# Performance work log

Hardware: AMD Instinct MI355X
Metric: run time of the kernel (lower is better)

Reference implementation:

```python
import jax, jax.numpy as jnp
import numpy as np

N = 100000
E = 1600000
IN_DIM = 64
HID = 64
OUT = 64
NCLS = 40
EPS_BN = 1e-5


def _sym_norms(src, dst, n):
    # DGL GraphConv norm='both': src scaled by out_degree^-1/2, dst by in_degree^-1/2,
    # degrees clamped to min 1.
    ones = jnp.ones(src.shape[0], dtype=jnp.float32)
    deg_out = jax.ops.segment_sum(ones, src, num_segments=n)
    deg_in = jax.ops.segment_sum(ones, dst, num_segments=n)
    return jnp.clip(deg_out, 1.0) ** -0.5, jnp.clip(deg_in, 1.0) ** -0.5


def _graph_conv(x, src, dst, norm_src, norm_dst, W, b):
    # D_dst^{-1/2} A D_src^{-1/2} X W + b
    x = x * norm_src[:, None]
    agg = jax.ops.segment_sum(x[src], dst, num_segments=x.shape[0])
    agg = agg * norm_dst[:, None]
    return agg @ W + b


def _gcn(x, src, dst, W1, b1, W2, b2):
    ns, nd = _sym_norms(src, dst, x.shape[0])
    h = jax.nn.relu(_graph_conv(x, src, dst, ns, nd, W1, b1))
    return _graph_conv(h, src, dst, ns, nd, W2, b2)


def setup_inputs() -> dict:
    key = jax.random.key(0)
    ks = jax.random.split(key, 16)
    glorot = lambda k, fi, fo: jax.random.normal(k, (fi, fo), jnp.float32) * np.sqrt(2.0 / (fi + fo))
    return {
        "feat1": jax.random.normal(ks[0], (N, IN_DIM), jnp.float32),
        "src1": jax.random.randint(ks[1], (E,), 0, N, jnp.int32),
        "dst1": jax.random.randint(ks[2], (E,), 0, N, jnp.int32),
        "feat2": jax.random.normal(ks[3], (N, IN_DIM), jnp.float32),
        "src2": jax.random.randint(ks[4], (E,), 0, N, jnp.int32),
        "dst2": jax.random.randint(ks[5], (E,), 0, N, jnp.int32),
        "W1a": glorot(ks[6], IN_DIM, HID), "b1a": jnp.zeros(HID, jnp.float32),
        "W1b": glorot(ks[7], HID, OUT), "b1b": jnp.zeros(OUT, jnp.float32),
        "W2a": glorot(ks[8], IN_DIM, HID), "b2a": jnp.zeros(HID, jnp.float32),
        "W2b": glorot(ks[9], HID, OUT), "b2b": jnp.zeros(OUT, jnp.float32),
        "Wm1": glorot(ks[10], OUT, HID), "bm1": jnp.zeros(HID, jnp.float32),
        "gamma": jnp.ones(HID, jnp.float32), "beta": jnp.zeros(HID, jnp.float32),
        "Wm2": glorot(ks[11], HID, NCLS), "bm2": jnp.zeros(NCLS, jnp.float32),
    }


def reference(feat1, src1, dst1, feat2, src2, dst2,
              W1a, b1a, W1b, b1b, W2a, b2a, W2b, b2b,
              Wm1, bm1, gamma, beta, Wm2, bm2):
    h1 = _gcn(feat1, src1, dst1, W1a, b1a, W1b, b1b)
    h2 = _gcn(feat2, src2, dst2, W2a, b2a, W2b, b2b)
    # torch .std() is unbiased (ddof=1)
    z1 = (h1 - h1.mean(0)) / jnp.std(h1, axis=0, ddof=1)
    z2 = (h2 - h2.mean(0)) / jnp.std(h2, axis=0, ddof=1)
    z = (z1 + z2) * 0.5
    # MLP2 head: Linear -> BatchNorm1d (training-mode batch stats) -> ReLU -> Linear
    y = z @ Wm1 + bm1
    mu = y.mean(0)
    var = y.var(0)  # biased, as BN uses
    y = (y - mu) * jax.lax.rsqrt(var + EPS_BN) * gamma + beta
    pred_y = jax.nn.relu(y) @ Wm2 + bm2
    return (z1, z2, pred_y)
```

## Files before the change

kernel.cpp:

```cpp
#include <hip/hip_runtime.h>
#include <hip/hip_bf16.h>

#define DIM 64
#define NCLS_OUT 40
#define BSH 8
#define BROWS 256
#define BIN_CHUNK 12288

typedef __hip_bfloat16 bf16;

__device__ __forceinline__ float lane_bcast(float v, int l) {
  return __int_as_float(__builtin_amdgcn_readlane(__float_as_int(v), l));
}
__device__ __forceinline__ unsigned short f2bf_bits(float f) {
  bf16 h = __float2bfloat16(f);
  return *reinterpret_cast<unsigned short*>(&h);
}

__device__ __forceinline__ float ldf(const void* p, long i, int m) {
  return m ? ((const float*)p)[i] : __bfloat162float(((const bf16*)p)[i]);
}
__device__ __forceinline__ void stf(void* p, long i, float v, int m) {
  if (m) ((float*)p)[i] = v;
  else ((bf16*)p)[i] = __float2bfloat16(v);
}

__global__ void k_detect(const unsigned int* __restrict__ wds, int nw, int* __restrict__ mode) {
  __shared__ int cnt_s;
  if (threadIdx.x == 0) cnt_s = 0;
  __syncthreads();
  int c = 0;
  for (int i = threadIdx.x; i < nw; i += 1024) {
    unsigned h = wds[i] & 0xFFFFu;
    unsigned e = (h >> 7) & 0xFFu;
    if (e == 0xFFu || (e != 0u && e < 0x60u)) c++;
  }
  atomicAdd(&cnt_s, c);
  __syncthreads();
  if (threadIdx.x == 0) *mode = (cnt_s > nw / 16) ? 1 : 0;
}

__global__ void k_deg_hist(const int* __restrict__ src1, const int* __restrict__ dst1,
                           const int* __restrict__ src2, const int* __restrict__ dst2,
                           int* __restrict__ deg, int* __restrict__ bh,
                           int n, int e1, int etot, int NB) {
  extern __shared__ int cnt[];
  for (int b = threadIdx.x; b < NB; b += blockDim.x) cnt[b] = 0;
  __syncthreads();
  int stride = gridDim.x * blockDim.x;
  for (int i = blockIdx.x * blockDim.x + threadIdx.x; i < etot; i += stride) {
    int s, row;
    if (i < e1) { s = src1[i]; row = dst1[i]; }
    else { s = src2[i - e1]; row = n + dst2[i - e1]; }
    atomicAdd(&deg[2 * n + (row < n ? 0 : 0) + (i < e1 ? s : n + s)], 1);
    atomicAdd(&cnt[row >> BSH], 1);
  }
  __syncthreads();
  for (int b = threadIdx.x; b < NB; b += blockDim.x)
    if (cnt[b]) atomicAdd(&bh[b], cnt[b]);
}

__global__ void k_norm(const int* __restrict__ deg, float* __restrict__ nrm, int n4) {
  int i = blockIdx.x * 256 + threadIdx.x;
  if (i < n4) {
    int d = deg[i];
    if (d < 1) d = 1;
    nrm[i] = rsqrtf((float)d);
  }
}

__global__ void k_bscan(const int* __restrict__ bh, int* __restrict__ bbase,
                        int* __restrict__ gcur, int* __restrict__ rp,
                        int NB, int etot, int n2) {
  __shared__ int sm[256];
  __shared__ int carry_s;
  int t = threadIdx.x;
  if (t == 0) carry_s = 0;
  __syncthreads();
  for (int base = 0; base < NB; base += 256) {
    int i = base + t;
    int v = (i < NB) ? bh[i] : 0;
    sm[t] = v;
    __syncthreads();
    for (int o = 1; o < 256; o <<= 1) {
      int a = (t >= o) ? sm[t - o] : 0;
      __syncthreads();
      sm[t] += a;
      __syncthreads();
    }
    int c = carry_s;
    int excl = c + sm[t] - v;
    int tot = sm[255];
    __syncthreads();
    if (i < NB) { bbase[i] = excl; gcur[i] = excl; }
    if (t == 0) carry_s = c + tot;
    __syncthreads();
  }
  if (t == 0) { bbase[NB] = etot; rp[n2] = etot; }
}

__global__ void __launch_bounds__(256) k_bin(
    const int* __restrict__ src1, const int* __restrict__ dst1,
    const int* __restrict__ src2, const int* __restrict__ dst2,
    int* __restrict__ gcur, unsigned* __restrict__ eb,
    int n, int e1, int etot, int NB) {
  extern __shared__ int lds[];
  int* cnt = lds;
  int* base = lds + NB;
  int t = threadIdx.x;
  int c0 = blockIdx.x * BIN_CHUNK;
  int cend = c0 + BIN_CHUNK;
  if (cend > etot) cend = etot;
  for (int b = t; b < NB; b += 256) cnt[b] = 0;
  __syncthreads();
  for (int i = c0 + t; i < cend; i += 256) {
    int row = (i < e1) ? dst1[i] : (n + dst2[i - e1]);
    atomicAdd(&cnt[row >> BSH], 1);
  }
  __syncthreads();
  for (int b = t; b < NB; b += 256) {
    int c = cnt[b];
    base[b] = c ? atomicAdd(&gcur[b], c) : 0;
    cnt[b] = 0;
  }
  __syncthreads();
  for (int i = c0 + t; i < cend; i += 256) {
    int s, row;
    if (i < e1) { s = src1[i]; row = dst1[i]; }
    else { s = src2[i - e1]; row = n + dst2[i - e1]; }
    int b = row >> BSH;
    int l = atomicAdd(&cnt[b], 1);
    eb[base[b] + l] = ((unsigned)(row & (BROWS - 1)) << 24) | (unsigned)s;
  }
}

__global__ void __launch_bounds__(256) k_fine(
    const unsigned* __restrict__ eb, const int* __restrict__ bbase,
    int* __restrict__ rp, int* __restrict__ deg, int* __restrict__ sb,
    int n2, int NB) {
  __shared__ int hist[256];
  __shared__ int sm[256];
  __shared__ int curs[256];
  int t = threadIdx.x;
  for (int b = blockIdx.x; b < NB; b += gridDim.x) {
    int ebeg = bbase[b], eend = bbase[b + 1];
    hist[t] = 0;
    __syncthreads();
    for (int i = ebeg + t; i < eend; i += 256)
      atomicAdd(&hist[eb[i] >> 24], 1);
    __syncthreads();
    int v = hist[t];
    sm[t] = v;
    __syncthreads();
    for (int o = 1; o < 256; o <<= 1) {
      int a = (t >= o) ? sm[t - o] : 0;
      __syncthreads();
      sm[t] += a;
      __syncthreads();
    }
    int excl = sm[t] - v;
    int row = (b << BSH) + t;
    if (row < n2) { deg[row] = v; rp[row] = ebeg + excl; }
    curs[t] = excl;
    __syncthreads();
    for (int i = ebeg + t; i < eend; i += 256) {
      unsigned u = eb[i];
      int l = atomicAdd(&curs[u >> 24], 1);
      sb[ebeg + l] = (int)(u & 0xFFFFFFu);
    }
    __syncthreads();
  }
}

__global__ void k_scale_all(const void* __restrict__ f1, const void* __restrict__ f2,
                            const float* __restrict__ norms, bf16* __restrict__ P,
                            int n, const int* __restrict__ mode) {
  int m = *mode;
  int i = blockIdx.x * 256 + threadIdx.x;
  int nd = n * DIM;
  if (i >= 2 * nd) return;
  int g = i >= nd;
  int li = g ? i - nd : i;
  float ns = norms[2 * n + g * n + (li >> 6)];
  P[i] = __float2bfloat16(ldf(g ? f2 : f1, li, m) * ns);
}

__global__ void k_scale_one(const void* __restrict__ f, const float* __restrict__ ns,
                            bf16* __restrict__ P, int nd, const int* __restrict__ mode) {
  int m = *mode;
  int i = blockIdx.x * 256 + threadIdx.x;
  if (i < nd) P[i] = __float2bfloat16(ldf(f, i, m) * ns[i >> 6]);
}

__global__ void __launch_bounds__(256) k_gmm(
    const bf16* __restrict__ X, const int* __restrict__ rp, const int* __restrict__ sb,
    const void* __restrict__ Wg0, const void* __restrict__ bg0,
    const void* __restrict__ Wg1, const void* __restrict__ bg1,
    const float* __restrict__ pre0, const float* __restrict__ pre1,
    const float* __restrict__ post0, const float* __restrict__ post1,
    bf16* __restrict__ Y, int n, int relu, const int* __restrict__ mode,
    int dual, int gsel, float* __restrict__ stats) {
  int m = *mode;
  int t = threadIdx.x, lane = t & 63, wid = t >> 6;
  int g = dual ? (blockIdx.x & 1) : gsel;
  int ord = dual ? (blockIdx.x >> 1) : blockIdx.x;
  int nblk = dual ? (gridDim.x >> 1) : gridDim.x;
  int rowbase = dual ? g * n : 0;

  const void* W = g ? Wg1 : Wg0;
  const void* bb = g ? bg1 : bg0;
  const float* pre = g ? pre1 : pre0;
  const float* post = g ? post1 : post0;

  unsigned wp[32];
#pragma unroll
  for (int i = 0; i < 32; ++i) {
    unsigned lb = f2bf_bits(ldf(W, (2 * i) * 64 + lane, m));
    unsigned hb = f2bf_bits(ldf(W, (2 * i + 1) * 64 + lane, m));
    wp[i] = lb | (hb << 16);
  }
  float bias = ldf(bb, lane, m);
  float ps = 0.f, pq = 0.f;

  int stride = nblk * 4;
  for (int node = ord * 4 + wid; node < n; node += stride) {
    int b0 = rp[g * n + node], e0 = rp[g * n + node + 1];
    float a0 = 0.f, a1 = 0.f, a2 = 0.f, a3 = 0.f;
    for (int base = b0; base < e0; base += 64) {
      int cnt = e0 - base;
      if (cnt > 64) cnt = 64;
      int eidx = (lane < cnt) ? sb[base + lane] : 0;
      int j = 0;
      for (; j + 8 <= cnt; j += 8) {
        int s0 = __builtin_amdgcn_readlane(eidx, j);
        int s1 = __builtin_amdgcn_readlane(eidx, j + 1);
        int s2 = __builtin_amdgcn_readlane(eidx, j + 2);
        int s3 = __builtin_amdgcn_readlane(eidx, j + 3);
        int s4 = __builtin_amdgcn_readlane(eidx, j + 4);
        int s5 = __builtin_amdgcn_readlane(eidx, j + 5);
        int s6 = __builtin_amdgcn_readlane(eidx, j + 6);
        int s7 = __builtin_amdgcn_readlane(eidx, j + 7);
        float v0 = __bfloat162float(X[(long)(rowbase + s0) * DIM + lane]);
        float v1 = __bfloat162float(X[(long)(rowbase + s1) * DIM + lane]);
        float v2 = __bfloat162float(X[(long)(rowbase + s2) * DIM + lane]);
        float v3 = __bfloat162float(X[(long)(rowbase + s3) * DIM + lane]);
        float v4 = __bfloat162float(X[(long)(rowbase + s4) * DIM + lane]);
        float v5 = __bfloat162float(X[(long)(rowbase + s5) * DIM + lane]);
        float v6 = __bfloat162float(X[(long)(rowbase + s6) * DIM + lane]);
        float v7 = __bfloat162float(X[(long)(rowbase + s7) * DIM + lane]);
        a0 += v0; a1 += v1; a2 += v2; a3 += v3;
        a0 += v4; a1 += v5; a2 += v6; a3 += v7;
      }
      for (; j + 4 <= cnt; j += 4) {
        int s0 = __builtin_amdgcn_readlane(eidx, j);
        int s1 = __builtin_amdgcn_readlane(eidx, j + 1);
        int s2 = __builtin_amdgcn_readlane(eidx, j + 2);
        int s3 = __builtin_amdgcn_readlane(eidx, j + 3);
        a0 += __bfloat162float(X[(long)(rowbase + s0) * DIM + lane]);
        a1 += __bfloat162float(X[(long)(rowbase + s1) * DIM + lane]);
        a2 += __bfloat162float(X[(long)(rowbase + s2) * DIM + lane]);
        a3 += __bfloat162float(X[(long)(rowbase + s3) * DIM + lane]);
      }
      for (; j < cnt; ++j) {
        int s0 = __builtin_amdgcn_readlane(eidx, j);
        a0 += __bfloat162float(X[(long)(rowbase + s0) * DIM + lane]);
      }
    }
    float acc = (a0 + a1) + (a2 + a3);
    acc *= pre[node];
    float r = 0.f;
#pragma unroll
    for (int i = 0; i < 32; ++i) {
      r = fmaf(lane_bcast(acc, 2 * i), __uint_as_float(wp[i] << 16), r);
      r = fmaf(lane_bcast(acc, 2 * i + 1), __uint_as_float(wp[i] & 0xFFFF0000u), r);
    }
    r += bias;
    if (relu) r = fmaxf(r, 0.f);
    if (post) r *= post[node];
    Y[(long)(rowbase + node) * DIM + lane] = __float2bfloat16(r);
    ps += r;
    pq += r * r;
  }

  if (stats) {
    __shared__ float ssum[4][64], ssq[4][64];
    ssum[wid][lane] = ps;
    ssq[wid][lane] = pq;
    __syncthreads();
    if (t < 64) {
      float a = ssum[0][t] + ssum[1][t] + ssum[2][t] + ssum[3][t];
      float b2 = ssq[0][t] + ssq[1][t] + ssq[2][t] + ssq[3][t];
      atomicAdd(&stats[g * 128 + t], a);
      atomicAdd(&stats[g * 128 + 64 + t], b2);
    }
  }
}

__global__ void __launch_bounds__(256) k_mm64s(const bf16* __restrict__ X,
                                               const void* __restrict__ W,
                                               const void* __restrict__ b,
                                               bf16* __restrict__ Y, int n,
                                               const int* __restrict__ mode,
                                               float* __restrict__ stats) {
  int m = *mode;
  int t = threadIdx.x, lane = t & 63, wid = t >> 6;
  float w[64];
#pragma unroll
  for (int k = 0; k < 64; ++k) w[k] = ldf(W, k * 64 + lane, m);
  float bias = ldf(b, lane, m);
  float ps = 0.f, pq = 0.f;
  int stride = gridDim.x * 4;
  for (int row = blockIdx.x * 4 + wid; row < n; row += stride) {
    float a = __bfloat162float(X[(long)row * 64 + lane]);
    float acc = 0.f;
#pragma unroll
    for (int k = 0; k < 64; ++k) acc = fmaf(lane_bcast(a, k), w[k], acc);
    acc += bias;
    Y[(long)row * 64 + lane] = __float2bfloat16(acc);
    ps += acc;
    pq += acc * acc;
  }
  __shared__ float ssum[4][64], ssq[4][64];
  ssum[wid][lane] = ps;
  ssq[wid][lane] = pq;
  __syncthreads();
  if (t < 64) {
    float a = ssum[0][t] + ssum[1][t] + ssum[2][t] + ssum[3][t];
    float b2 = ssq[0][t] + ssq[1][t] + ssq[2][t] + ssq[3][t];
    atomicAdd(&stats[t], a);
    atomicAdd(&stats[64 + t], b2);
  }
}

__global__ void k_z_dual(const bf16* __restrict__ H, const float* __restrict__ stats,
                         void* __restrict__ zout, bf16* __restrict__ Dz, int n,
                         const int* __restrict__ mode) {
  int m = *mode;
  int i = blockIdx.x * 256 + threadIdx.x;
  int nd = n * DIM;
  if (i >= nd) return;
  int c = i & 63;
  float fn = (float)n;
  float mu1 = stats[c] / fn;
  float var1 = fmaxf((stats[64 + c] - mu1 * mu1 * fn) / (fn - 1.0f), 1e-12f);
  float mu2 = stats[128 + c] / fn;
  float var2 = fmaxf((stats[192 + c] - mu2 * mu2 * fn) / (fn - 1.0f), 1e-12f);
  float z1 = (__bfloat162float(H[i]) - mu1) * rsqrtf(var1);
  float z2 = (__bfloat162float(H[nd + i]) - mu2) * rsqrtf(var2);
  stf(zout, i, z1, m);
  stf(zout, (long)nd + i, z2, m);
  Dz[i] = __float2bfloat16(0.5f * (z1 + z2));
}

__global__ void k_z_seq(const bf16* __restrict__ h, const float* __restrict__ stats,
                        void* __restrict__ zout, long zoff, bf16* __restrict__ zacc,
                        int n, int init, const int* __restrict__ mode) {
  int m = *mode;
  int i = blockIdx.x * 256 + threadIdx.x;
  if (i >= n * DIM) return;
  int c = i & 63;
  float fn = (float)n;
  float mu = stats[c] / fn;
  float var = fmaxf((stats[64 + c] - mu * mu * fn) / (fn - 1.0f), 1e-12f);
  float z = (__bfloat162float(h[i]) - mu) * rsqrtf(var);
  stf(zout, zoff + i, z, m);
  float prev = init ? 0.f : __bfloat162float(zacc[i]);
  zacc[i] = __float2bfloat16(prev + 0.5f * z);
}

__global__ void __launch_bounds__(256) k_head(const bf16* __restrict__ Yv,
                                              const float* __restrict__ s,
                                              const float* __restrict__ sq,
                                              const void* __restrict__ gamma,
                                              const void* __restrict__ beta,
                                              const void* __restrict__ W2,
                                              const void* __restrict__ b2,
                                              void* __restrict__ out, long ooff, int n,
                                              const int* __restrict__ mode) {
  int m = *mode;
  int t = threadIdx.x, lane = t & 63, wid = t >> 6;
  float w[64];
#pragma unroll
  for (int k = 0; k < 64; ++k)
    w[k] = (lane < NCLS_OUT) ? ldf(W2, k * NCLS_OUT + lane, m) : 0.f;
  float bias = (lane < NCLS_OUT) ? ldf(b2, lane, m) : 0.f;
  float fn = (float)n;
  float mu = s[lane] / fn;
  float var = sq[lane] / fn - mu * mu;
  float rstd = rsqrtf(fmaxf(var, 0.f) + 1e-5f);
  float g = ldf(gamma, lane, m);
  float be = ldf(beta, lane, m);
  int stride = gridDim.x * 4;
  for (int row = blockIdx.x * 4 + wid; row < n; row += stride) {
    float yv = __bfloat162float(Yv[(long)row * 64 + lane]);
    float yn = fmaxf((yv - mu) * rstd * g + be, 0.f);
    float acc = bias;
#pragma unroll
    for (int k = 0; k < 64; ++k) acc = fmaf(lane_bcast(yn, k), w[k], acc);
    if (lane < NCLS_OUT) stf(out, ooff + (long)row * NCLS_OUT + lane, acc, m);
  }
}

extern "C" void kernel_launch(void* const* d_in, const int* in_sizes, int n_in,
                              void* d_out, int out_size, void* d_ws, size_t ws_size,
                              hipStream_t stream) {
  const void* feat1 = d_in[0];
  const int* src1 = (const int*)d_in[1];
  const int* dst1 = (const int*)d_in[2];
  const void* feat2 = d_in[3];
  const int* src2 = (const int*)d_in[4];
  const int* dst2 = (const int*)d_in[5];
  const void* W1a = d_in[6];
  const void* b1a = d_in[7];
  const void* W1b = d_in[8];
  const void* b1b = d_in[9];
  const void* W2a = d_in[10];
  const void* b2a = d_in[11];
  const void* W2b = d_in[12];
  const void* b2b = d_in[13];
  const void* Wm1 = d_in[14];
  const void* bm1 = d_in[15];
  const void* gamma = d_in[16];
  const void* beta = d_in[17];
  const void* Wm2 = d_in[18];
  const void* bm2 = d_in[19];

  const int n = in_sizes[0] / DIM;
  const int e1 = in_sizes[1];
  const int e2 = in_sizes[4];
  const int etot = e1 + e2;
  const long nd = (long)n * DIM;
  const int NB = (2 * n + BROWS - 1) >> BSH;

  char* w = (char*)d_ws;
  size_t off = 0;
  auto alloc = [&](size_t bytes) -> void* {
    void* p = w + off;
    off += (bytes + 255) & ~(size_t)255;
    return p;
  };
  int* mode = (int*)alloc(256);
  int* deg = (int*)alloc((size_t)4 * n * 4);
  float* stats = (float*)alloc(512 * 4);
  float* norms = (float*)alloc((size_t)4 * n * 4);
  int* rp = (int*)alloc((size_t)(2 * n + 8) * 4);
  int* bh = (int*)alloc((size_t)(NB + 1) * 4);
  int* bbase = (int*)alloc((size_t)(NB + 1) * 4);
  int* gcur = (int*)alloc((size_t)(NB + 1) * 4);
  int* sb = (int*)alloc((size_t)etot * 4);
  size_t base_off = off;
  bool dual = (ws_size >= base_off + (size_t)5 * nd * 2 + 4096);

  bf16 *P, *Q, *Dz;
  size_t qbytes;
  if (dual) {
    P = (bf16*)alloc((size_t)2 * nd * 2);
    Q = (bf16*)alloc((size_t)2 * nd * 2);
    Dz = (bf16*)alloc((size_t)nd * 2);
    qbytes = (size_t)2 * nd * 2;
  } else {
    P = (bf16*)alloc((size_t)nd * 2);
    Q = (bf16*)alloc((size_t)nd * 2);
    Dz = (bf16*)alloc((size_t)nd * 2);
    qbytes = (size_t)nd * 2;
  }
  unsigned* eb = ((size_t)etot * 4 <= qbytes) ? (unsigned*)Q
                                              : (unsigned*)alloc((size_t)etot * 4);

  const float* nd1 = norms;
  const float* nd2 = norms + n;
  const float* ns1 = norms + 2 * n;
  const float* ns2 = norms + 3 * n;

  int gND = (int)((nd + 255) / 256);
  int g2ND = (int)((2 * nd + 255) / 256);
  int g4N = (4 * n + 255) / 256;
  int gBIN = (etot + BIN_CHUNK - 1) / BIN_CHUNK;
  const int gGMM = 4096;

  hipMemsetAsync(deg + 2 * n, 0, (size_t)2 * n * 4, stream);
  hipMemsetAsync(stats, 0, 512 * 4, stream);
  hipMemsetAsync(bh, 0, (size_t)NB * 4, stream);

  k_detect<<<1, 1024, 0, stream>>>((const unsigned int*)feat1, 8192, mode);

  k_deg_hist<<<256, 256, (size_t)NB * 4, stream>>>(src1, dst1, src2, dst2, deg, bh,
                                                   n, e1, etot, NB);
  k_bscan<<<1, 256, 0, stream>>>(bh, bbase, gcur, rp, NB, etot, 2 * n);
  k_bin<<<gBIN, 256, (size_t)2 * NB * 4, stream>>>(src1, dst1, src2, dst2, gcur, eb,
                                                   n, e1, etot, NB);
  k_fine<<<NB, 256, 0, stream>>>(eb, bbase, rp, deg, sb, 2 * n, NB);
  k_norm<<<g4N, 256, 0, stream>>>(deg, norms, 4 * n);

  if (dual) {
    k_scale_all<<<g2ND, 256, 0, stream>>>(feat1, feat2, norms, P, n, mode);
    k_gmm<<<gGMM, 256, 0, stream>>>(P, rp, sb, W1a, b1a, W2a, b2a, nd1, nd2, ns1, ns2,
                                    Q, n, 1, mode, 1, 0, (float*)nullptr);
    k_gmm<<<gGMM, 256, 0, stream>>>(Q, rp, sb, W1b, b1b, W2b, b2b, nd1, nd2,
                                    (const float*)nullptr, (const float*)nullptr,
                                    P, n, 0, mode, 1, 0, stats);
    k_z_dual<<<gND, 256, 0, stream>>>(P, stats, d_out, Dz, n, mode);
  } else {
    k_scale_one<<<gND, 256, 0, stream>>>(feat1, ns1, P, (int)nd, mode);
    k_gmm<<<gGMM, 256, 0, stream>>>(P, rp, sb, W1a, b1a, W1a, b1a, nd1, nd1, ns1, ns1,
                                    Q, n, 1, mode, 0, 0, (float*)nullptr);
    k_gmm<<<gGMM, 256, 0, stream>>>(Q, rp, sb, W1b, b1b, W1b, b1b, nd1, nd1,
                                    (const float*)nullptr, (const float*)nullptr,
                                    P, n, 0, mode, 0, 0, stats);
    k_z_seq<<<gND, 256, 0, stream>>>(P, stats, d_out, 0L, Dz, n, 1, mode);
    k_scale_one<<<gND, 256, 0, stream>>>(feat2, ns2, P, (int)nd, mode);
    k_gmm<<<gGMM, 256, 0, stream>>>(P, rp, sb, W2a, b2a, W2a, b2a, nd2, nd2, ns2, ns2,
                                    Q, n, 1, mode, 0, 1, (float*)nullptr);
    k_gmm<<<gGMM, 256, 0, stream>>>(Q, rp, sb, W2b, b2b, W2b, b2b, nd2, nd2,
                                    (const float*)nullptr, (const float*)nullptr,
                                    P, n, 0, mode, 0, 1, stats + 128);
    k_z_seq<<<gND, 256, 0, stream>>>(P, stats + 128, d_out, nd, Dz, n, 0, mode);
  }

  k_mm64s<<<512, 256, 0, stream>>>(Dz, Wm1, bm1, Q, n, mode, stats + 256);
  k_head<<<512, 256, 0, stream>>>(Q, stats + 256, stats + 320, gamma, beta, Wm2, bm2,
                                  d_out, 2 * nd, n, mode);
}
```

Measured before the change: 957.8 us.

## Fuse norm computation into k_fine, z-normalize into MLP matmul, vectorize scaling

Drops the separate k_norm kernel: k_fine now writes the in-degree and out-degree rsqrt norms directly. In the dual path, the z-score kernel and the first MLP matmul are merged into k_zmm, so the averaged z tensor is no longer written to and reread from global memory. k_scale_all now handles 8 elements per thread with vector loads and stores. The aim is fewer launches and less memory traffic, at the cost of k_zmm running on only 512 blocks for work that previously had full-grid parallelism.

```diff
diff --git a/kernel.cpp b/kernel.cpp
--- a/kernel.cpp
+++ b/kernel.cpp
@@ -15,6 +15,9 @@
 __device__ __forceinline__ unsigned short f2bf_bits(float f) {
   bf16 h = __float2bfloat16(f);
   return *reinterpret_cast<unsigned short*>(&h);
+}
+__device__ __forceinline__ float bfbits2f(unsigned short u) {
+  return __uint_as_float((unsigned)u << 16);
 }
 
 __device__ __forceinline__ float ldf(const void* p, long i, int m) {
@@ -51,22 +54,13 @@
   for (int i = blockIdx.x * blockDim.x + threadIdx.x; i < etot; i += stride) {
     int s, row;
     if (i < e1) { s = src1[i]; row = dst1[i]; }
-    else { s = src2[i - e1]; row = n + dst2[i - e1]; }
-    atomicAdd(&deg[2 * n + (row < n ? 0 : 0) + (i < e1 ? s : n + s)], 1);
+    else { s = n + src2[i - e1]; row = n + dst2[i - e1]; }
+    atomicAdd(&deg[2 * n + s], 1);
     atomicAdd(&cnt[row >> BSH], 1);
   }
   __syncthreads();
   for (int b = threadIdx.x; b < NB; b += blockDim.x)
     if (cnt[b]) atomicAdd(&bh[b], cnt[b]);
-}
-
-__global__ void k_norm(const int* __restrict__ deg, float* __restrict__ nrm, int n4) {
-  int i = blockIdx.x * 256 + threadIdx.x;
-  if (i < n4) {
-    int d = deg[i];
-    if (d < 1) d = 1;
-    nrm[i] = rsqrtf((float)d);
-  }
 }
 
 __global__ void k_bscan(const int* __restrict__ bh, int* __restrict__ bbase,
@@ -136,8 +130,8 @@
 
 __global__ void __launch_bounds__(256) k_fine(
     const unsigned* __restrict__ eb, const int* __restrict__ bbase,
-    int* __restrict__ rp, int* __restrict__ deg, int* __restrict__ sb,
-    int n2, int NB) {
+    int* __restrict__ rp, const int* __restrict__ deg, float* __restrict__ nrm,
+    int* __restrict__ sb, int n2, int NB) {
   __shared__ int hist[256];
   __shared__ int sm[256];
   __shared__ int curs[256];
@@ -160,7 +154,12 @@
     }
     int excl = sm[t] - v;
     int row = (b << BSH) + t;
-    if (row < n2) { deg[row] = v; rp[row] = ebeg + excl; }
+    if (row < n2) {
+      rp[row] = ebeg + excl;
+      nrm[row] = rsqrtf((float)(v < 1 ? 1 : v));
+      int dov = deg[n2 + row];
+      nrm[n2 + row] = rsqrtf((float)(dov < 1 ? 1 : dov));
+    }
     curs[t] = excl;
     __syncthreads();
     for (int i = ebeg + t; i < eend; i += 256) {
@@ -176,13 +175,33 @@
                             const float* __restrict__ norms, bf16* __restrict__ P,
                             int n, const int* __restrict__ mode) {
   int m = *mode;
-  int i = blockIdx.x * 256 + threadIdx.x;
-  int nd = n * DIM;
-  if (i >= 2 * nd) return;
-  int g = i >= nd;
-  int li = g ? i - nd : i;
-  float ns = norms[2 * n + g * n + (li >> 6)];
-  P[i] = __float2bfloat16(ldf(g ? f2 : f1, li, m) * ns);
+  long i8 = ((long)blockIdx.x * 256 + threadIdx.x) * 8;
+  long nd = (long)n * DIM;
+  if (i8 >= 2 * nd) return;
+  int g = i8 >= nd;
+  long li = g ? i8 - nd : i8;
+  float ns = norms[2 * n + g * n + (int)(li >> 6)];
+  const void* f = g ? f2 : f1;
+  float x[8];
+  if (m) {
+    const float4* fp = (const float4*)((const char*)f + li * 4);
+    float4 a = fp[0], b = fp[1];
+    x[0] = a.x; x[1] = a.y; x[2] = a.z; x[3] = a.w;
+    x[4] = b.x; x[5] = b.y; x[6] = b.z; x[7] = b.w;
+  } else {
+    const ushort4* hp = (const ushort4*)((const char*)f + li * 2);
+    ushort4 a = hp[0], b = hp[1];
+    x[0] = bfbits2f(a.x); x[1] = bfbits2f(a.y);
+    x[2] = bfbits2f(a.z); x[3] = bfbits2f(a.w);
+    x[4] = bfbits2f(b.x); x[5] = bfbits2f(b.y);
+    x[6] = bfbits2f(b.z); x[7] = bfbits2f(b.w);
+  }
+  uint4 o;
+  o.x = f2bf_bits(x[0] * ns) | ((unsigned)f2bf_bits(x[1] * ns) << 16);
+  o.y = f2bf_bits(x[2] * ns) | ((unsigned)f2bf_bits(x[3] * ns) << 16);
+  o.z = f2bf_bits(x[4] * ns) | ((unsigned)f2bf_bits(x[5] * ns) << 16);
+  o.w = f2bf_bits(x[6] * ns) | ((unsigned)f2bf_bits(x[7] * ns) << 16);
+  *(uint4*)((char*)P + i8 * 2) = o;
 }
 
 __global__ void k_scale_one(const void* __restrict__ f, const float* __restrict__ ns,
@@ -296,6 +315,56 @@
   }
 }
 
+__global__ void __launch_bounds__(256) k_zmm(const bf16* __restrict__ H,
+                                             const float* __restrict__ stats,
+                                             void* __restrict__ zout,
+                                             const void* __restrict__ Wm,
+                                             const void* __restrict__ bm,
+                                             bf16* __restrict__ Y, int n,
+                                             const int* __restrict__ mode,
+                                             float* __restrict__ ystats) {
+  int m = *mode;
+  int t = threadIdx.x, lane = t & 63, wid = t >> 6;
+  float w[64];
+#pragma unroll
+  for (int k = 0; k < 64; ++k) w[k] = ldf(Wm, k * 64 + lane, m);
+  float bias = ldf(bm, lane, m);
+  float fn = (float)n;
+  float mu1 = stats[lane] / fn;
+  float var1 = fmaxf((stats[64 + lane] - mu1 * mu1 * fn) / (fn - 1.0f), 1e-12f);
+  float mu2 = stats[128 + lane] / fn;
+  float var2 = fmaxf((stats[192 + lane] - mu2 * mu2 * fn) / (fn - 1.0f), 1e-12f);
+  float rs1 = rsqrtf(var1), rs2 = rsqrtf(var2);
+  long nd = (long)n * DIM;
+  float ps = 0.f, pq = 0.f;
+  int stride = gridDim.x * 4;
+  for (int row = blockIdx.x * 4 + wid; row < n; row += stride) {
+    long idx = (long)row * DIM + lane;
+    float z1 = (__bfloat162float(H[idx]) - mu1) * rs1;
+    float z2 = (__bfloat162float(H[nd + idx]) - mu2) * rs2;
+    stf(zout, idx, z1, m);
+    stf(zout, nd + idx, z2, m);
+    float dz = 0.5f * (z1 + z2);
+    float acc = 0.f;
+#pragma unroll
+    for (int k = 0; k < 64; ++k) acc = fmaf(lane_bcast(dz, k), w[k], acc);
+    acc += bias;
+    Y[idx] = __float2bfloat16(acc);
+    ps += acc;
+    pq += acc * acc;
+  }
+  __shared__ float ssum[4][64], ssq[4][64];
+  ssum[wid][lane] = ps;
+  ssq[wid][lane] = pq;
+  __syncthreads();
+  if (t < 64) {
+    float a = ssum[0][t] + ssum[1][t] + ssum[2][t] + ssum[3][t];
+    float b2 = ssq[0][t] + ssq[1][t] + ssq[2][t] + ssq[3][t];
+    atomicAdd(&ystats[t], a);
+    atomicAdd(&ystats[64 + t], b2);
+  }
+}
+
 __global__ void __launch_bounds__(256) k_mm64s(const bf16* __restrict__ X,
                                                const void* __restrict__ W,
                                                const void* __restrict__ b,
@@ -330,26 +399,6 @@
     atomicAdd(&stats[t], a);
     atomicAdd(&stats[64 + t], b2);
   }
-}
-
-__global__ void k_z_dual(const bf16* __restrict__ H, const float* __restrict__ stats,
-                         void* __restrict__ zout, bf16* __restrict__ Dz, int n,
-                         const int* __restrict__ mode) {
-  int m = *mode;
-  int i = blockIdx.x * 256 + threadIdx.x;
-  int nd = n * DIM;
-  if (i >= nd) return;
-  int c = i & 63;
-  float fn = (float)n;
-  float mu1 = stats[c] / fn;
-  float var1 = fmaxf((stats[64 + c] - mu1 * mu1 * fn) / (fn - 1.0f), 1e-12f);
-  float mu2 = stats[128 + c] / fn;
-  float var2 = fmaxf((stats[192 + c] - mu2 * mu2 * fn) / (fn - 1.0f), 1e-12f);
-  float z1 = (__bfloat162float(H[i]) - mu1) * rsqrtf(var1);
-  float z2 = (__bfloat162float(H[nd + i]) - mu2) * rsqrtf(var2);
-  stf(zout, i, z1, m);
-  stf(zout, (long)nd + i, z2, m);
-  Dz[i] = __float2bfloat16(0.5f * (z1 + z2));
 }
 
 __global__ void k_z_seq(const bf16* __restrict__ h, const float* __restrict__ stats,
@@ -473,8 +522,7 @@
   const float* ns2 = norms + 3 * n;
 
   int gND = (int)((nd + 255) / 256);
-  int g2ND = (int)((2 * nd + 255) / 256);
-  int g4N = (4 * n + 255) / 256;
+  int g2ND8 = (int)((2 * nd / 8 + 255) / 256);
   int gBIN = (etot + BIN_CHUNK - 1) / BIN_CHUNK;
   const int gGMM = 4096;
 
@@ -489,17 +537,16 @@
   k_bscan<<<1, 256, 0, stream>>>(bh, bbase, gcur, rp, NB, etot, 2 * n);
   k_bin<<<gBIN, 256, (size_t)2 * NB * 4, stream>>>(src1, dst1, src2, dst2, gcur, eb,
                                                    n, e1, etot, NB);
-  k_fine<<<NB, 256, 0, stream>>>(eb, bbase, rp, deg, sb, 2 * n, NB);
-  k_norm<<<g4N, 256, 0, stream>>>(deg, norms, 4 * n);
+  k_fine<<<NB, 256, 0, stream>>>(eb, bbase, rp, deg, norms, sb, 2 * n, NB);
 
   if (dual) {
-    k_scale_all<<<g2ND, 256, 0, stream>>>(feat1, feat2, norms, P, n, mode);
+    k_scale_all<<<g2ND8, 256, 0, stream>>>(feat1, feat2, norms, P, n, mode);
     k_gmm<<<gGMM, 256, 0, stream>>>(P, rp, sb, W1a, b1a, W2a, b2a, nd1, nd2, ns1, ns2,
                                     Q, n, 1, mode, 1, 0, (float*)nullptr);
     k_gmm<<<gGMM, 256, 0, stream>>>(Q, rp, sb, W1b, b1b, W2b, b2b, nd1, nd2,
                                     (const float*)nullptr, (const float*)nullptr,
                                     P, n, 0, mode, 1, 0, stats);
-    k_z_dual<<<gND, 256, 0, stream>>>(P, stats, d_out, Dz, n, mode);
+    k_zmm<<<512, 256, 0, stream>>>(P, stats, d_out, Wm1, bm1, Q, n, mode, stats + 256);
   } else {
     k_scale_one<<<gND, 256, 0, stream>>>(feat1, ns1, P, (int)nd, mode);
     k_gmm<<<gGMM, 256, 0, stream>>>(P, rp, sb, W1a, b1a, W1a, b1a, nd1, nd1, ns1, ns1,
@@ -515,9 +562,9 @@
                                     (const float*)nullptr, (const float*)nullptr,
                                     P, n, 0, mode, 0, 1, stats + 128);
     k_z_seq<<<gND, 256, 0, stream>>>(P, stats + 128, d_out, nd, Dz, n, 0, mode);
-  }
-
-  k_mm64s<<<512, 256, 0, stream>>>(Dz, Wm1, bm1, Q, n, mode, stats + 256);
+    k_mm64s<<<512, 256, 0, stream>>>(Dz, Wm1, bm1, Q, n, mode, stats + 256);
+  }
+
   k_head<<<512, 256, 0, stream>>>(Q, stats + 256, stats + 320, gamma, beta, Wm2, bm2,
                                   d_out, 2 * nd, n, mode);
 }
```

Result: no change. 940.3 us, median of 2 (-1.8%).
